# Performance work log

Hardware: AMD Instinct MI355X
Metric: run time of the kernel (lower is better)

Reference implementation:

```python
import jax, jax.numpy as jnp
import numpy as np

H = 224; W = 224; ZNEAR = 0.01; ZFAR = 100.0; EPS2D = 0.3
N_GAUSS = 1024; N_CAM = 2
ALPHA_MIN = 1.0 / 255.0; ALPHA_MAX = 0.999


def quat_to_rotmat(q):
    # gsplat convention: wxyz, normalized internally. q: [N,4] -> [N,3,3]
    q = q / jnp.linalg.norm(q, axis=-1, keepdims=True)
    w, x, y, z = q[:, 0], q[:, 1], q[:, 2], q[:, 3]
    R = jnp.stack([
        jnp.stack([1.0 - 2.0 * (y * y + z * z), 2.0 * (x * y - w * z), 2.0 * (x * z + w * y)], -1),
        jnp.stack([2.0 * (x * y + w * z), 1.0 - 2.0 * (x * x + z * z), 2.0 * (y * z - w * x)], -1),
        jnp.stack([2.0 * (x * z - w * y), 2.0 * (y * z + w * x), 1.0 - 2.0 * (x * x + y * y)], -1),
    ], -2)
    return R


def setup_inputs() -> dict:
    key = jax.random.key(0)
    ks = jax.random.split(key, 5)
    xyz = jax.random.normal(ks[0], (N_GAUSS, 3), dtype=jnp.float32) * 0.5
    rgb = jax.random.uniform(ks[1], (N_GAUSS, 3), dtype=jnp.float32)
    opacity = jax.random.uniform(ks[2], (N_GAUSS,), dtype=jnp.float32)
    scale = jax.random.uniform(ks[3], (N_GAUSS, 3), dtype=jnp.float32) * 0.04 + 0.005
    rotation = jax.random.normal(ks[4], (N_GAUSS, 4), dtype=jnp.float32)
    w2c_list = []
    for a in (0.0, 0.3):  # two views, small yaw apart, camera 3 units back
        c, s = np.cos(a), np.sin(a)
        w2c_list.append(np.array([[c, 0, -s, 0], [0, 1, 0, 0], [s, 0, c, 3.0], [0, 0, 0, 1]], dtype=np.float32))
    w2cs = jnp.asarray(np.stack(w2c_list))
    K = np.array([[300.0, 0.0, 112.0], [0.0, 300.0, 112.0], [0.0, 0.0, 1.0]], dtype=np.float32)
    Ks = jnp.asarray(np.stack([K] * N_CAM))
    return {"w2cs": w2cs, "Ks": Ks, "xyz": xyz, "rgb": rgb, "opacity": opacity, "scale": scale, "rotation": rotation}


def _render_one(viewmat, K, means, cov3d, colors, opac, bg):
    R = viewmat[:3, :3]; t = viewmat[:3, 3]
    p_cam = means @ R.T + t                       # [N,3]
    z = p_cam[:, 2]; rz = 1.0 / z
    fx, fy, cx, cy = K[0, 0], K[1, 1], K[0, 2], K[1, 2]
    lim_x = 1.3 * (0.5 * W / fx); lim_y = 1.3 * (0.5 * H / fy)
    tx = z * jnp.clip(p_cam[:, 0] * rz, -lim_x, lim_x)
    ty = z * jnp.clip(p_cam[:, 1] * rz, -lim_y, lim_y)
    # camera-frame 3D covariance, then perspective Jacobian projection to 2D
    cov_cam = jnp.einsum('ij,njk,lk->nil', R, cov3d, R)   # [N,3,3]
    zero = jnp.zeros_like(rz)
    J = jnp.stack([
        jnp.stack([fx * rz, zero, -fx * tx * rz * rz], -1),
        jnp.stack([zero, fy * rz, -fy * ty * rz * rz], -1),
    ], -2)                                                # [N,2,3]
    cov2d = jnp.einsum('nij,njk,nlk->nil', J, cov_cam, J) # [N,2,2]
    a = cov2d[:, 0, 0] + EPS2D; d = cov2d[:, 1, 1] + EPS2D; b = cov2d[:, 0, 1]
    det = a * d - b * b
    ia = d / det; id_ = a / det; ib = -b / det            # inverse of blurred 2D cov
    u = fx * p_cam[:, 0] * rz + cx
    v = fy * p_cam[:, 1] * rz + cy
    valid = (z > ZNEAR) & (z < ZFAR) & (det > 0)
    o = jnp.where(valid, opac, 0.0)
    # front-to-back depth sort (gradients flow through gathered values)
    order = jnp.argsort(z)
    u, v, ia, ib, id_, o = (arr[order] for arr in (u, v, ia, ib, id_, o))
    colors_s = colors[order]
    # pixel centers, row-major flattened grid [P]
    xs = jnp.arange(W, dtype=jnp.float32) + 0.5
    ys = jnp.arange(H, dtype=jnp.float32) + 0.5
    pix_x = jnp.tile(xs, H); pix_y = jnp.repeat(ys, W)
    dx = u[None, :] - pix_x[:, None]                      # [P,N]
    dy = v[None, :] - pix_y[:, None]
    sigma = 0.5 * (ia * dx * dx + id_ * dy * dy) + ib * dx * dy
    alpha = jnp.minimum(o[None, :] * jnp.exp(-sigma), ALPHA_MAX)
    alpha = jnp.where((sigma >= 0.0) & (alpha > ALPHA_MIN), alpha, 0.0)
    log1m = jnp.log1p(-alpha)
    logT = jnp.cumsum(log1m, axis=1)
    T = jnp.exp(logT - log1m)                             # exclusive transmittance
    wgt = alpha * T                                       # [P,N]
    img = wgt @ colors_s                                  # [P,3]
    Tf = jnp.exp(logT[:, -1])
    img = img + Tf[:, None] * bg
    return img.reshape(H, W, 3), (1.0 - Tf).reshape(H, W, 1)


def reference(w2cs, Ks, xyz, rgb, opacity, scale, rotation):
    Rq = quat_to_rotmat(rotation)                         # [N,3,3]
    M = Rq * scale[:, None, :]                            # R @ diag(s)
    cov3d = jnp.einsum('nij,nkj->nik', M, M)              # R S S^T R^T
    bg = jnp.ones((3,), dtype=xyz.dtype)                  # bg_color buffer of ones
    imgs, alphas = jax.vmap(lambda vm, K: _render_one(vm, K, xyz, cov3d, rgb, opacity, bg))(w2cs, Ks)
    return imgs, alphas                                   # rgb [C,H,W,3], mask [C,H,W,1]
```

## Files before the change

### kernel.cpp

```cpp
#include <hip/hip_runtime.h>
#include <math.h>

#define NG 1024
#define NC 2
#define HH 224
#define WW 224
#define TILES_X 28
#define TILES_Y 28
#define EPS2D 0.3f
#define ALPHA_MIN (1.0f/255.0f)
#define ALPHA_MAX 0.999f
#define MAXL 512

__global__ __launch_bounds__(256) void fused_kernel(
        const float* __restrict__ w2cs, const float* __restrict__ Ks,
        const float* __restrict__ xyz, const float* __restrict__ rgb,
        const float* __restrict__ opac, const float* __restrict__ scale,
        const float* __restrict__ rot, float* __restrict__ out) {
    const int cam = blockIdx.z;
    const int TX = blockIdx.x, TY = blockIdx.y;
    const int tid = threadIdx.x;
    const int lane = tid & 63;
    const int wv   = tid >> 6;

    __shared__ unsigned long long keys[MAXL];
    __shared__ float4 sA[MAXL];
    __shared__ float4 sB[MAXL];
    __shared__ float  sC[MAXL];
    __shared__ float4 part[4][64];
    __shared__ int scnt;

    if (tid == 0) scnt = 0;
    __syncthreads();

    const float* vm = w2cs + cam*16;
    const float R00 = vm[0],  R01 = vm[1],  R02 = vm[2],  t0 = vm[3];
    const float R10 = vm[4],  R11 = vm[5],  R12 = vm[6],  t1 = vm[7];
    const float R20 = vm[8],  R21 = vm[9],  R22 = vm[10], t2 = vm[11];
    const float* Kc = Ks + cam*9;
    const float fx = Kc[0], cx = Kc[2], fy = Kc[4], cy = Kc[5];
    const float limx = 1.3f * (0.5f * (float)WW / fx);
    const float limy = 1.3f * (0.5f * (float)HH / fy);

    #pragma unroll
    for (int k = 0; k < 4; k++) {
        int g = k*256 + tid;
        float X = xyz[g*3], Y = xyz[g*3+1], Z = xyz[g*3+2];
        float pz = R20*X + R21*Y + R22*Z + t2;
        float o  = opac[g];
        float tau = __logf(255.f * o);
        bool cand = (pz > 0.01f) && (pz < 100.f) && (tau > 0.f);
        if (cand) {
            float rz = 1.f / pz;
            float px = R00*X + R01*Y + R02*Z + t0;
            float py = R10*X + R11*Y + R12*Z + t1;
            float u = fx*px*rz + cx;
            float v = fy*py*rz + cy;
            float sx = scale[g*3+0], sy = scale[g*3+1], sz = scale[g*3+2];
            float smax = fmaxf(sx, fmaxf(sy, sz));
            float j00 = fx*rz, j11 = fy*rz;
            float j02m = fx*limx*rz, j12m = fy*limy*rz;
            float abnd = smax*smax*(j00*j00 + j02m*j02m) + EPS2D;
            float dbnd = smax*smax*(j11*j11 + j12m*j12m) + EPS2D;
            float rx = sqrtf(2.f*tau*abnd) + 0.01f;
            float ry = sqrtf(2.f*tau*dbnd) + 0.01f;
            int xmin = max((int)ceilf (u - rx - 0.5f), 0);
            int xmax = min((int)floorf(u + rx - 0.5f), WW-1);
            int ymin = max((int)ceilf (v - ry - 0.5f), 0);
            int ymax = min((int)floorf(v + ry - 0.5f), HH-1);
            cand = (xmin <= xmax) && (ymin <= ymax) &&
                   (TX >= (xmin>>3)) && (TX <= (xmax>>3)) &&
                   (TY >= (ymin>>3)) && (TY <= (ymax>>3));
            if (cand) {
                unsigned long long m = __ballot(true);
                (void)m;
            }
        }
        unsigned long long m = __ballot(cand);
        int cw = __popcll(m);
        if (cw) {
            int basepos = 0;
            if (lane == 0) basepos = atomicAdd(&scnt, cw);
            basepos = __shfl(basepos, 0);
            if (cand) {
                float zz = R20*X + R21*Y + R22*Z + t2;
                int pos = basepos + __popcll(m & ((1ull << lane) - 1ull));
                if (pos < MAXL)
                    keys[pos] = ((unsigned long long)__float_as_uint(zz) << 10)
                              | (unsigned long long)g;
            }
        }
    }
    __syncthreads();
    int n = min(scnt, MAXL);

    int P = 2; while (P < n) P <<= 1;
    for (int i = tid; i < P; i += 256) if (i >= n) keys[i] = ~0ull;
    __syncthreads();
    for (int kk = 2; kk <= P; kk <<= 1) {
        for (int j = kk >> 1; j > 0; j >>= 1) {
            for (int i0 = tid; i0 < P; i0 += 256) {
                int ixj = i0 ^ j;
                if (ixj > i0) {
                    unsigned long long a = keys[i0], b = keys[ixj];
                    bool up = ((i0 & kk) == 0);
                    if ((a > b) == up) { keys[i0] = b; keys[ixj] = a; }
                }
            }
            __syncthreads();
        }
    }

    for (int i = tid; i < n; i += 256) {
        int g = (int)(keys[i] & 1023ull);

        float qw = rot[g*4+0], qx = rot[g*4+1], qy = rot[g*4+2], qz = rot[g*4+3];
        float qn = rsqrtf(qw*qw + qx*qx + qy*qy + qz*qz);
        qw *= qn; qx *= qn; qy *= qn; qz *= qn;
        float r00 = 1.f - 2.f*(qy*qy + qz*qz), r01 = 2.f*(qx*qy - qw*qz), r02 = 2.f*(qx*qz + qw*qy);
        float r10 = 2.f*(qx*qy + qw*qz), r11 = 1.f - 2.f*(qx*qx + qz*qz), r12 = 2.f*(qy*qz - qw*qx);
        float r20 = 2.f*(qx*qz - qw*qy), r21 = 2.f*(qy*qz + qw*qx), r22 = 1.f - 2.f*(qx*qx + qy*qy);

        float sx = scale[g*3+0], sy = scale[g*3+1], sz = scale[g*3+2];
        float m00 = r00*sx, m01 = r01*sy, m02 = r02*sz;
        float m10 = r10*sx, m11 = r11*sy, m12 = r12*sz;
        float m20 = r20*sx, m21 = r21*sy, m22 = r22*sz;
        float c00 = m00*m00 + m01*m01 + m02*m02;
        float c01 = m00*m10 + m01*m11 + m02*m12;
        float c02 = m00*m20 + m01*m21 + m02*m22;
        float c11 = m10*m10 + m11*m11 + m12*m12;
        float c12 = m10*m20 + m11*m21 + m12*m22;
        float c22 = m20*m20 + m21*m21 + m22*m22;

        float X = xyz[g*3], Y = xyz[g*3+1], Z = xyz[g*3+2];
        float px = R00*X + R01*Y + R02*Z + t0;
        float py = R10*X + R11*Y + R12*Z + t1;
        float pz = R20*X + R21*Y + R22*Z + t2;
        float rz = 1.f / pz;

        float txc = pz * fminf(fmaxf(px*rz, -limx), limx);
        float tyc = pz * fminf(fmaxf(py*rz, -limy), limy);

        float v00 = R00*c00 + R01*c01 + R02*c02;
        float v01 = R00*c01 + R01*c11 + R02*c12;
        float v02 = R00*c02 + R01*c12 + R02*c22;
        float v10 = R10*c00 + R11*c01 + R12*c02;
        float v11 = R10*c01 + R11*c11 + R12*c12;
        float v12 = R10*c02 + R11*c12 + R12*c22;
        float v20 = R20*c00 + R21*c01 + R22*c02;
        float v21 = R20*c01 + R21*c11 + R22*c12;
        float v22 = R20*c02 + R21*c12 + R22*c22;
        float cc00 = v00*R00 + v01*R01 + v02*R02;
        float cc01 = v00*R10 + v01*R11 + v02*R12;
        float cc02 = v00*R20 + v01*R21 + v02*R22;
        float cc11 = v10*R10 + v11*R11 + v12*R12;
        float cc12 = v10*R20 + v11*R21 + v12*R22;
        float cc22 = v20*R20 + v21*R21 + v22*R22;

        float j00 = fx*rz, j02 = -fx*txc*rz*rz;
        float j11 = fy*rz, j12 = -fy*tyc*rz*rz;
        float a = j00*j00*cc00 + 2.f*j00*j02*cc02 + j02*j02*cc22 + EPS2D;
        float bq = j00*j11*cc01 + j00*j12*cc02 + j02*j11*cc12 + j02*j12*cc22;
        float d = j11*j11*cc11 + 2.f*j11*j12*cc12 + j12*j12*cc22 + EPS2D;
        float det = a*d - bq*bq;

        bool valid = (pz > 0.01f) && (pz < 100.f) && (det > 0.f);
        float idet = valid ? (1.f / det) : 0.f;
        float ia  = d * idet;
        float ib  = -bq * idet;
        float id_ = a * idet;
        float u = valid ? (fx*px*rz + cx) : 0.f;
        float v = valid ? (fy*py*rz + cy) : 0.f;
        float o = valid ? opac[g] : 0.f;

        sA[i] = make_float4(u, v, ia, ib);
        sB[i] = make_float4(id_, o, rgb[g*3+0], rgb[g*3+1]);
        sC[i] = rgb[g*3+2];
    }
    __syncthreads();

    const float pxl = (float)(TX*8 + (lane & 7)) + 0.5f;
    const float pyl = (float)(TY*8 + (lane >> 3)) + 0.5f;
    int seglen = (n + 3) >> 2;
    int js = wv * seglen;
    int je = min(n, js + seglen);

    float T = 1.f, cr = 0.f, cg = 0.f, cb = 0.f;
    for (int j = js; j < je; j++) {
        float4 ga = sA[j];
        float4 gb = sB[j];
        float  bv = sC[j];
        float dx = ga.x - pxl;
        float dy = ga.y - pyl;
        float sigma = 0.5f*(ga.z*dx*dx + gb.x*dy*dy) + ga.w*dx*dy;
        float alpha = fminf(gb.y * __expf(-sigma), ALPHA_MAX);
        alpha = (sigma >= 0.f && alpha > ALPHA_MIN) ? alpha : 0.f;
        float w = alpha * T;
        cr += w * gb.z;
        cg += w * gb.w;
        cb += w * bv;
        T  -= alpha * T;
        if (((j - js) & 15) == 15 && __all(T < 1e-4f)) break;
    }

    part[wv][lane] = make_float4(cr, cg, cb, T);
    __syncthreads();

    if (tid < 64) {
        float4 c0 = part[0][lane];
        float Cr = c0.x, Cg = c0.y, Cb = c0.z, Tp = c0.w;
        #pragma unroll
        for (int s = 1; s < 4; s++) {
            float4 cs = part[s][lane];
            Cr += Tp * cs.x;
            Cg += Tp * cs.y;
            Cb += Tp * cs.z;
            Tp *= cs.w;
        }
        int p = (TY*8 + (lane >> 3)) * WW + TX*8 + (lane & 7);
        float* img = out + (size_t)cam * (HH*WW*3) + (size_t)p * 3;
        img[0] = Cr + Tp;
        img[1] = Cg + Tp;
        img[2] = Cb + Tp;
        out[(size_t)NC*HH*WW*3 + (size_t)cam*(HH*WW) + p] = 1.f - Tp;
    }
}

extern "C" void kernel_launch(void* const* d_in, const int* in_sizes, int n_in,
                              void* d_out, int out_size, void* d_ws, size_t ws_size,
                              hipStream_t stream) {
    const float* w2cs  = (const float*)d_in[0];
    const float* Ks    = (const float*)d_in[1];
    const float* xyz   = (const float*)d_in[2];
    const float* rgb   = (const float*)d_in[3];
    const float* opac  = (const float*)d_in[4];
    const float* scale = (const float*)d_in[5];
    const float* rot   = (const float*)d_in[6];
    float* out = (float*)d_out;

    fused_kernel<<<dim3(TILES_X, TILES_Y, NC), 256, 0, stream>>>(
        w2cs, Ks, xyz, rgb, opac, scale, rot, out);
}
```

Measured before the change: 81.18 us.

## Replace bitonic sort with rank sort, cull gaussians per tile, use exp2

Result: faster. 77.94 us, median of 2 (-4.0%).

```diff
diff --git a/kernel.cpp b/kernel.cpp
--- a/kernel.cpp
+++ b/kernel.cpp
@@ -11,6 +11,7 @@
 #define ALPHA_MIN (1.0f/255.0f)
 #define ALPHA_MAX 0.999f
 #define MAXL 512
+#define LOG2E 1.4426950408889634f
 
 __global__ __launch_bounds__(256) void fused_kernel(
         const float* __restrict__ w2cs, const float* __restrict__ Ks,
@@ -23,12 +24,15 @@
     const int lane = tid & 63;
     const int wv   = tid >> 6;
 
-    __shared__ unsigned long long keys[MAXL];
+    __shared__ union {
+        unsigned long long keys[MAXL];
+        float4 part[4][64];
+    } shu;
     __shared__ float4 sA[MAXL];
     __shared__ float4 sB[MAXL];
     __shared__ float  sC[MAXL];
-    __shared__ float4 part[4][64];
-    __shared__ int scnt;
+    __shared__ int    cnt[8];
+    __shared__ int    scnt;
 
     if (tid == 0) scnt = 0;
     __syncthreads();
@@ -54,8 +58,8 @@
             float rz = 1.f / pz;
             float px = R00*X + R01*Y + R02*Z + t0;
             float py = R10*X + R11*Y + R12*Z + t1;
-            float u = fx*px*rz + cx;
-            float v = fy*py*rz + cy;
+            float uu = fx*px*rz + cx;
+            float vv = fy*py*rz + cy;
             float sx = scale[g*3+0], sy = scale[g*3+1], sz = scale[g*3+2];
             float smax = fmaxf(sx, fmaxf(sy, sz));
             float j00 = fx*rz, j11 = fy*rz;
@@ -64,17 +68,13 @@
             float dbnd = smax*smax*(j11*j11 + j12m*j12m) + EPS2D;
             float rx = sqrtf(2.f*tau*abnd) + 0.01f;
             float ry = sqrtf(2.f*tau*dbnd) + 0.01f;
-            int xmin = max((int)ceilf (u - rx - 0.5f), 0);
-            int xmax = min((int)floorf(u + rx - 0.5f), WW-1);
-            int ymin = max((int)ceilf (v - ry - 0.5f), 0);
-            int ymax = min((int)floorf(v + ry - 0.5f), HH-1);
+            int xmin = max((int)ceilf (uu - rx - 0.5f), 0);
+            int xmax = min((int)floorf(uu + rx - 0.5f), WW-1);
+            int ymin = max((int)ceilf (vv - ry - 0.5f), 0);
+            int ymax = min((int)floorf(vv + ry - 0.5f), HH-1);
             cand = (xmin <= xmax) && (ymin <= ymax) &&
                    (TX >= (xmin>>3)) && (TX <= (xmax>>3)) &&
                    (TY >= (ymin>>3)) && (TY <= (ymax>>3));
-            if (cand) {
-                unsigned long long m = __ballot(true);
-                (void)m;
-            }
         }
         unsigned long long m = __ballot(cand);
         int cw = __popcll(m);
@@ -83,36 +83,33 @@
             if (lane == 0) basepos = atomicAdd(&scnt, cw);
             basepos = __shfl(basepos, 0);
             if (cand) {
-                float zz = R20*X + R21*Y + R22*Z + t2;
                 int pos = basepos + __popcll(m & ((1ull << lane) - 1ull));
                 if (pos < MAXL)
-                    keys[pos] = ((unsigned long long)__float_as_uint(zz) << 10)
-                              | (unsigned long long)g;
+                    shu.keys[pos] = ((unsigned long long)__float_as_uint(pz) << 10)
+                                  | (unsigned long long)g;
             }
         }
     }
     __syncthreads();
     int n = min(scnt, MAXL);
 
-    int P = 2; while (P < n) P <<= 1;
-    for (int i = tid; i < P; i += 256) if (i >= n) keys[i] = ~0ull;
-    __syncthreads();
-    for (int kk = 2; kk <= P; kk <<= 1) {
-        for (int j = kk >> 1; j > 0; j >>= 1) {
-            for (int i0 = tid; i0 < P; i0 += 256) {
-                int ixj = i0 ^ j;
-                if (ixj > i0) {
-                    unsigned long long a = keys[i0], b = keys[ixj];
-                    bool up = ((i0 & kk) == 0);
-                    if ((a > b) == up) { keys[i0] = b; keys[ixj] = a; }
-                }
-            }
-            __syncthreads();
-        }
-    }
-
-    for (int i = tid; i < n; i += 256) {
-        int g = (int)(keys[i] & 1023ull);
+    unsigned long long myk0 = (tid       < n) ? shu.keys[tid]       : 0ull;
+    unsigned long long myk1 = (tid + 256 < n) ? shu.keys[tid + 256] : 0ull;
+    int r0 = 0, r1 = 0;
+    #pragma unroll 4
+    for (int j = 0; j < n; j++) {
+        unsigned long long kj = shu.keys[j];
+        r0 += (kj < myk0) ? 1 : 0;
+        r1 += (kj < myk1) ? 1 : 0;
+    }
+    __syncthreads();
+    if (tid       < n) shu.keys[r0] = myk0;
+    if (tid + 256 < n) shu.keys[r1] = myk1;
+    __syncthreads();
+
+    auto prep = [&](int i, float4 &A, float4 &B, float &C) -> bool {
+        if (i >= n) return false;
+        int g = (int)(shu.keys[i] & 1023ull);
 
         float qw = rot[g*4+0], qx = rot[g*4+1], qy = rot[g*4+2], qz = rot[g*4+3];
         float qn = rsqrtf(qw*qw + qx*qx + qy*qy + qz*qz);
@@ -159,59 +156,93 @@
 
         float j00 = fx*rz, j02 = -fx*txc*rz*rz;
         float j11 = fy*rz, j12 = -fy*tyc*rz*rz;
-        float a = j00*j00*cc00 + 2.f*j00*j02*cc02 + j02*j02*cc22 + EPS2D;
+        float a  = j00*j00*cc00 + 2.f*j00*j02*cc02 + j02*j02*cc22 + EPS2D;
         float bq = j00*j11*cc01 + j00*j12*cc02 + j02*j11*cc12 + j02*j12*cc22;
-        float d = j11*j11*cc11 + 2.f*j11*j12*cc12 + j12*j12*cc22 + EPS2D;
+        float d  = j11*j11*cc11 + 2.f*j11*j12*cc12 + j12*j12*cc22 + EPS2D;
         float det = a*d - bq*bq;
 
-        bool valid = (pz > 0.01f) && (pz < 100.f) && (det > 0.f);
-        float idet = valid ? (1.f / det) : 0.f;
-        float ia  = d * idet;
-        float ib  = -bq * idet;
-        float id_ = a * idet;
-        float u = valid ? (fx*px*rz + cx) : 0.f;
-        float v = valid ? (fy*py*rz + cy) : 0.f;
-        float o = valid ? opac[g] : 0.f;
-
-        sA[i] = make_float4(u, v, ia, ib);
-        sB[i] = make_float4(id_, o, rgb[g*3+0], rgb[g*3+1]);
-        sC[i] = rgb[g*3+2];
-    }
+        if (!((pz > 0.01f) && (pz < 100.f) && (det > 0.f))) return false;
+
+        float o = opac[g];
+        float tau = __logf(255.f * o);
+        if (!(tau > 0.f)) return false;
+
+        float hx = sqrtf(2.f*tau*a) + 0.02f;
+        float hy = sqrtf(2.f*tau*d) + 0.02f;
+        float uu = fx*px*rz + cx;
+        float vv = fy*py*rz + cy;
+        float xlo = (float)(TX*8) + 0.5f, xhi = (float)(TX*8) + 7.5f;
+        float ylo = (float)(TY*8) + 0.5f, yhi = (float)(TY*8) + 7.5f;
+        if (uu + hx < xlo || uu - hx > xhi || vv + hy < ylo || vv - hy > yhi)
+            return false;
+
+        float idet = 1.f / det;
+        A = make_float4(uu, vv, 0.5f*LOG2E*d*idet, -LOG2E*bq*idet);
+        B = make_float4(0.5f*LOG2E*a*idet, o, rgb[g*3+0], rgb[g*3+1]);
+        C = rgb[g*3+2];
+        return true;
+    };
+
+    float4 A0, B0, A1, B1; float C0, C1;
+    bool kp0 = prep(tid,       A0, B0, C0);
+    bool kp1 = prep(tid + 256, A1, B1, C1);
+
+    unsigned long long bal0 = __ballot(kp0);
+    unsigned long long bal1 = __ballot(kp1);
+    if (lane == 0) { cnt[wv] = __popcll(bal0); cnt[4 + wv] = __popcll(bal1); }
+    __syncthreads();
+    int base0 = 0, base1 = 0, n2 = 0;
+    #pragma unroll
+    for (int s = 0; s < 8; s++) {
+        int cs = cnt[s];
+        base0 += (s < wv)     ? cs : 0;
+        base1 += (s < 4 + wv) ? cs : 0;
+        n2 += cs;
+    }
+    unsigned long long lt = (1ull << lane) - 1ull;
+    int d0 = base0 + __popcll(bal0 & lt);
+    int d1 = base1 + __popcll(bal1 & lt);
+    if (kp0) { sA[d0] = A0; sB[d0] = B0; sC[d0] = C0; }
+    if (kp1) { sA[d1] = A1; sB[d1] = B1; sC[d1] = C1; }
     __syncthreads();
 
     const float pxl = (float)(TX*8 + (lane & 7)) + 0.5f;
     const float pyl = (float)(TY*8 + (lane >> 3)) + 0.5f;
-    int seglen = (n + 3) >> 2;
+    int seglen = (n2 + 3) >> 2;
     int js = wv * seglen;
-    int je = min(n, js + seglen);
+    int je = min(n2, js + seglen);
 
     float T = 1.f, cr = 0.f, cg = 0.f, cb = 0.f;
-    for (int j = js; j < je; j++) {
-        float4 ga = sA[j];
-        float4 gb = sB[j];
-        float  bv = sC[j];
-        float dx = ga.x - pxl;
-        float dy = ga.y - pyl;
-        float sigma = 0.5f*(ga.z*dx*dx + gb.x*dy*dy) + ga.w*dx*dy;
-        float alpha = fminf(gb.y * __expf(-sigma), ALPHA_MAX);
-        alpha = (sigma >= 0.f && alpha > ALPHA_MIN) ? alpha : 0.f;
-        float w = alpha * T;
-        cr += w * gb.z;
-        cg += w * gb.w;
-        cb += w * bv;
-        T  -= alpha * T;
-        if (((j - js) & 15) == 15 && __all(T < 1e-4f)) break;
-    }
-
-    part[wv][lane] = make_float4(cr, cg, cb, T);
+#define CBODY(J) do { \
+        float4 ga = sA[J]; float4 gb = sB[J]; float bv = sC[J]; \
+        float dx = ga.x - pxl, dy = ga.y - pyl; \
+        float sg = ga.z*dx*dx + gb.x*dy*dy + ga.w*dx*dy; \
+        float al = fminf(gb.y * exp2f(-sg), ALPHA_MAX); \
+        al = (sg >= 0.f && al > ALPHA_MIN) ? al : 0.f; \
+        float wgt = al * T; \
+        cr += wgt * gb.z; cg += wgt * gb.w; cb += wgt * bv; \
+        T -= al * T; \
+    } while (0)
+
+    int j = js;
+    while (j + 16 <= je) {
+        #pragma unroll 4
+        for (int q = 0; q < 16; q++) { CBODY(j + q); }
+        j += 16;
+        if (__all(T < 1e-4f)) break;
+    }
+    for (; j < je; j++) { CBODY(j); }
+#undef CBODY
+
+    shu.part[wv][lane] = make_float4(cr, cg, cb, T);
     __syncthreads();
 
     if (tid < 64) {
-        float4 c0 = part[0][lane];
+        float4 c0 = shu.part[0][lane];
         float Cr = c0.x, Cg = c0.y, Cb = c0.z, Tp = c0.w;
         #pragma unroll
         for (int s = 1; s < 4; s++) {
-            float4 cs = part[s][lane];
+            float4 cs = shu.part[s][lane];
             Cr += Tp * cs.x;
             Cg += Tp * cs.y;
             Cb += Tp * cs.z;
```
